# Kernel tuning notes

Measured on AMD Instinct MI355X. Metric: run time of the kernel, lower is better.

The kernel has to match this reference:

```python
import jax, jax.numpy as jnp
import numpy as np

U = 512  # units

def hard_sigmoid(x):
    # Keras hard_sigmoid: clip(0.2*x + 0.5, 0, 1)
    return jnp.clip(0.2 * x + 0.5, 0.0, 1.0)

def setup_inputs() -> dict:
    key = jax.random.key(0)
    ks = jax.random.split(key, 9)
    B, T, A, D = 64, 2048, 512, 512  # batch, annotation steps, annotation units, input dim
    s = lambda k, shape, scale: jax.random.normal(k, shape, jnp.float32) * scale
    return {
        "inputs": s(ks[0], (B, D), 1.0),
        "h": s(ks[1], (B, U), 1.0),
        "c": s(ks[2], (B, U), 1.0),
        "annotations": s(ks[3], (B, T, A), 1.0),
        "kernel": s(ks[4], (D + A, 4 * U), 0.02),
        "recurrent_kernel": s(ks[5], (U, 4 * U), 0.02),
        "bias": jnp.zeros((6 * U,), jnp.float32).at[U:2 * U].set(1.0),  # unit_forget_bias
        "kernel_u": s(ks[6], (A, U), 0.02),
        "kernel_w": s(ks[7], (U, U), 0.02),
        "kernel_v": s(ks[8], (U,), 0.02),
    }

def reference(inputs, h, c, annotations, kernel, recurrent_kernel, bias, kernel_u, kernel_w, kernel_v):
    bias_u = bias[4 * U:5 * U]
    # precomputed annotation projection (done once in build()): [B,T,U]
    uh = jnp.einsum('bta,au->btu', annotations, kernel_u) + bias_u
    # Bahdanau attention scores
    Wxstm = h @ kernel_w                                   # [B,U]
    et = jnp.einsum('btu,u->bt', jnp.tanh(uh + Wxstm[:, None, :]), kernel_v)
    at = jax.nn.softmax(et, axis=1)                        # exp/sum in source == softmax
    context = jnp.einsum('bt,bta->ba', at, annotations)    # [B,A]
    x = jnp.concatenate([inputs, context], axis=-1)        # [B, D+A]
    z = x @ kernel + h @ recurrent_kernel + bias[:4 * U]   # [B,4U]
    i = hard_sigmoid(z[:, :U])
    f = hard_sigmoid(z[:, U:2 * U])
    c_new = f * c + i * jnp.tanh(z[:, 2 * U:3 * U])
    o = hard_sigmoid(z[:, 3 * U:])
    h_new = o * jnp.tanh(c_new)
    return h_new
```

## Files before the change

kernel.cpp:

```cpp
#include <hip/hip_runtime.h>

constexpr int U = 512;
constexpr int B = 64;
constexpr int T = 2048;
constexpr int A = 512;

typedef __attribute__((ext_vector_type(8))) short short8;
typedef __attribute__((ext_vector_type(4))) float f32x4;

__device__ __forceinline__ unsigned short f32_to_bf16(float f) {
    unsigned int b = __float_as_uint(f);
    unsigned int r = (b + 0x7FFFu + ((b >> 16) & 1u)) >> 16;
    return (unsigned short)r;
}

__device__ __forceinline__ float fast_tanh(float x) {
    float e = exp2f(x * 2.885390081777927f);
    return (e - 1.0f) * __builtin_amdgcn_rcpf(e + 1.0f);
}

__device__ __forceinline__ float hard_sigmoid(float z) {
    return fminf(fmaxf(0.2f * z + 0.5f, 0.0f), 1.0f);
}

__global__ __launch_bounds__(256) void k_prep_s(const float* __restrict__ h,
                                                const float* __restrict__ kw,
                                                float* __restrict__ Sp) {
    int b = blockIdx.x >> 2;
    int kc = blockIdx.x & 3;
    int u = threadIdx.x;
    const float* hb = h + b * U + kc * 128;
    const float* kwb = kw + (size_t)kc * 128 * U;
    float a0 = 0.f, a1 = 0.f;
#pragma unroll 4
    for (int k = 0; k < 128; ++k) {
        float hv = hb[k];
        a0 += hv * kwb[(size_t)k * U + u];
        a1 += hv * kwb[(size_t)k * U + u + 256];
    }
    float* p = Sp + ((size_t)kc * 64 + b) * U;
    p[u] = a0;
    p[u + 256] = a1;
}

__global__ __launch_bounds__(256) void k_s_reduce(const float* __restrict__ Sp,
                                                  const float* __restrict__ bias,
                                                  float* __restrict__ S) {
    int gid = blockIdx.x * 256 + threadIdx.x;
    int b = gid >> 9, u = gid & 511;
    float s = bias[4 * U + u];
#pragma unroll
    for (int kc = 0; kc < 4; ++kc) s += Sp[((size_t)kc * 64 + b) * U + u];
    S[gid] = s;
}

__global__ __launch_bounds__(256) void k_prep_kpack(const float* __restrict__ ku,
                                                    unsigned short* __restrict__ kpack) {
    int t = blockIdx.x >> 1;
    int u = (blockIdx.x & 1) * 256 + threadIdx.x;
    float vals[32];
#pragma unroll
    for (int j = 0; j < 32; ++j) vals[j] = ku[(size_t)(t * 32 + j) * U + u];
    unsigned short* out = kpack + (size_t)t * 16384 + u * 32;
    int ux = (u >> 1) & 3;
#pragma unroll
    for (int d = 0; d < 4; ++d) {
        int sc = d ^ ux;
        short8 pk;
#pragma unroll
        for (int e = 0; e < 8; ++e) pk[e] = (short)f32_to_bf16(vals[d * 8 + e]);
        *(short8*)&out[sc * 8] = pk;
    }
}

__global__ __launch_bounds__(256) void k_prep_wt(const float* __restrict__ kern,
                                                 const float* __restrict__ rk,
                                                 unsigned short* __restrict__ Wt) {
    __shared__ float tile[32][33];
    int k0 = blockIdx.x << 5;
    int j0 = blockIdx.y << 5;
    int c = threadIdx.x & 31, r0 = threadIdx.x >> 5;
#pragma unroll
    for (int p = 0; p < 4; ++p) {
        int r = r0 + p * 8;
        int k = k0 + r;
        float val = (k < 1024) ? kern[k * 2048 + j0 + c]
                               : rk[(k - 1024) * 2048 + j0 + c];
        tile[r][c] = val;
    }
    __syncthreads();
#pragma unroll
    for (int p = 0; p < 4; ++p) {
        int r = r0 + p * 8;
        Wt[(size_t)(j0 + r) * 1536 + k0 + c] = f32_to_bf16(tile[c][r]);
    }
}

__global__ __launch_bounds__(256, 2) void k_gemm_et(const float* __restrict__ ann,
                                                    const unsigned short* __restrict__ kpack,
                                                    const float* __restrict__ S,
                                                    const float* __restrict__ v,
                                                    float* __restrict__ et) {
    __shared__ unsigned short As[2][64 * 32];
    __shared__ unsigned short Bs[2][512 * 32];
    __shared__ float red[4][64];

    const int tid = threadIdx.x;
    const int wave = tid >> 6;
    const int lane = tid & 63;
    const int lanelo = lane & 15;
    const int quad = lane >> 4;
    const int wn = wave;

    const int mt = blockIdx.x;
    const int b = mt >> 5;
    const int t0 = (mt & 31) << 6;
    const float* aBase = ann + (size_t)mt * 64 * A;
    const char* kpB = (const char*)kpack;

    f32x4 acc[4][8];
#pragma unroll
    for (int i = 0; i < 4; ++i)
#pragma unroll
        for (int j = 0; j < 8; ++j) acc[i][j] = {0.f, 0.f, 0.f, 0.f};

    const int rowA = tid >> 2;
    const int c8A = tid & 3;
    f32x4 pv0, pv1;

    auto stage_b = [&](int t, int buf) {
        const char* src = kpB + (size_t)t * 32768;
#pragma unroll
        for (int p = 0; p < 8; ++p) {
            int seg = p * 4 + wave;
            __builtin_amdgcn_global_load_lds(
                (const __attribute__((address_space(1))) void*)(src + seg * 1024 + lane * 16),
                (__attribute__((address_space(3))) void*)((char*)&Bs[buf][0] + seg * 1024),
                16, 0, 0);
        }
    };

    auto cvt_store = [&](int buf) {
        short8 pk;
        pk[0] = (short)f32_to_bf16(pv0.x);
        pk[1] = (short)f32_to_bf16(pv0.y);
        pk[2] = (short)f32_to_bf16(pv0.z);
        pk[3] = (short)f32_to_bf16(pv0.w);
        pk[4] = (short)f32_to_bf16(pv1.x);
        pk[5] = (short)f32_to_bf16(pv1.y);
        pk[6] = (short)f32_to_bf16(pv1.z);
        pk[7] = (short)f32_to_bf16(pv1.w);
        *(short8*)&As[buf][rowA * 32 + ((c8A ^ ((rowA >> 1) & 3)) * 8)] = pk;
    };

    {
        const float* src = aBase + (size_t)rowA * A + c8A * 8;
        pv0 = *(const f32x4*)src;
        pv1 = *(const f32x4*)(src + 4);
    }
    stage_b(0, 0);
    cvt_store(0);
    __syncthreads();

    for (int t = 0; t < 16; ++t) {
        const int cur = t & 1;
        const int nxt = cur ^ 1;
        const bool more = (t < 15);

        if (more) {
            const float* src = aBase + (size_t)rowA * A + (t + 1) * 32 + c8A * 8;
            pv0 = *(const f32x4*)src;
            pv1 = *(const f32x4*)(src + 4);
            stage_b(t + 1, nxt);
        }

        short8 af[4];
#pragma unroll
        for (int mi = 0; mi < 4; ++mi) {
            int row = mi * 16 + lanelo;
            af[mi] = *(const short8*)&As[cur][row * 32 + ((quad ^ ((row >> 1) & 3)) * 8)];
        }
        short8 bfr[8];
#pragma unroll
        for (int ni = 0; ni < 8; ++ni) {
            int rowb = wn * 128 + ni * 16 + lanelo;
            bfr[ni] = *(const short8*)&Bs[cur][rowb * 32 + ((quad ^ ((rowb >> 1) & 3)) * 8)];
        }
        __builtin_amdgcn_s_setprio(1);
#pragma unroll
        for (int mi = 0; mi < 4; ++mi)
#pragma unroll
            for (int ni = 0; ni < 8; ++ni)
                acc[mi][ni] = __builtin_amdgcn_mfma_f32_16x16x32_bf16(
                    af[mi], bfr[ni], acc[mi][ni], 0, 0, 0);
        __builtin_amdgcn_s_setprio(0);

        if (more) {
            cvt_store(nxt);
        }
        __syncthreads();
    }

    float rows[16];
#pragma unroll
    for (int i = 0; i < 16; ++i) rows[i] = 0.f;
#pragma unroll
    for (int ni = 0; ni < 8; ++ni) {
        int u = wn * 128 + ni * 16 + lanelo;
        float sv = S[b * U + u];
        float vv = v[u];
#pragma unroll
        for (int mi = 0; mi < 4; ++mi)
#pragma unroll
            for (int r = 0; r < 4; ++r)
                rows[mi * 4 + r] += fast_tanh(acc[mi][ni][r] + sv) * vv;
    }
#pragma unroll
    for (int i = 0; i < 16; ++i) {
        rows[i] += __shfl_xor(rows[i], 1);
        rows[i] += __shfl_xor(rows[i], 2);
        rows[i] += __shfl_xor(rows[i], 4);
        rows[i] += __shfl_xor(rows[i], 8);
    }
    if (lanelo == 0) {
#pragma unroll
        for (int mi = 0; mi < 4; ++mi)
#pragma unroll
            for (int r = 0; r < 4; ++r)
                red[wave][mi * 16 + quad * 4 + r] = rows[mi * 4 + r];
    }
    __syncthreads();
    if (tid < 64) {
        float sum = red[0][tid] + red[1][tid] + red[2][tid] + red[3][tid];
        et[b * T + t0 + tid] = sum;
    }
}

__global__ __launch_bounds__(256) void k_softmax(const float* __restrict__ et,
                                                 float* __restrict__ at) {
    __shared__ float sred[256];
    int b = blockIdx.x;
    const float* e = et + b * T;
    float vals[8];
    float mx = -1e30f;
#pragma unroll
    for (int i = 0; i < 8; ++i) {
        int t = threadIdx.x + i * 256;
        float x = e[t];
        vals[i] = x;
        mx = fmaxf(mx, x);
    }
    sred[threadIdx.x] = mx;
    __syncthreads();
    for (int s = 128; s > 0; s >>= 1) {
        if (threadIdx.x < s) sred[threadIdx.x] = fmaxf(sred[threadIdx.x], sred[threadIdx.x + s]);
        __syncthreads();
    }
    mx = sred[0];
    __syncthreads();
    float sum = 0.f;
#pragma unroll
    for (int i = 0; i < 8; ++i) {
        float x = exp2f((vals[i] - mx) * 1.4426950408889634f);
        vals[i] = x;
        sum += x;
    }
    sred[threadIdx.x] = sum;
    __syncthreads();
    for (int s = 128; s > 0; s >>= 1) {
        if (threadIdx.x < s) sred[threadIdx.x] += sred[threadIdx.x + s];
        __syncthreads();
    }
    float inv = 1.0f / sred[0];
#pragma unroll
    for (int i = 0; i < 8; ++i) at[b * T + threadIdx.x + i * 256] = vals[i] * inv;
}

__global__ __launch_bounds__(256) void k_ctx_part(const float* __restrict__ at,
                                                  const float* __restrict__ ann,
                                                  float* __restrict__ part) {
    __shared__ float buf[2][512];
    int b = blockIdx.x >> 4;
    int tc = blockIdx.x & 15;
    int half = threadIdx.x >> 7;
    int a4 = (threadIdx.x & 127) << 2;
    const float* annb = ann + ((size_t)b * T + tc * 128) * A;
    const float* atb = at + b * T + tc * 128;
    f32x4 acc = {0.f, 0.f, 0.f, 0.f};
#pragma unroll 4
    for (int t = half; t < 128; t += 2) {
        float w = atb[t];
        f32x4 rv = *(const f32x4*)(annb + (size_t)t * A + a4);
        acc.x += w * rv.x;
        acc.y += w * rv.y;
        acc.z += w * rv.z;
        acc.w += w * rv.w;
    }
    *(f32x4*)&buf[half][a4] = acc;
    __syncthreads();
    int a2 = threadIdx.x << 1;
    float s0 = buf[0][a2] + buf[1][a2];
    float s1 = buf[0][a2 + 1] + buf[1][a2 + 1];
    float* p = part + ((size_t)b * 16 + tc) * A;
    p[a2] = s0;
    p[a2 + 1] = s1;
}

__global__ __launch_bounds__(256) void k_ctx_xb(const float* __restrict__ part,
                                                const float* __restrict__ inputs,
                                                const float* __restrict__ h,
                                                unsigned short* __restrict__ xb) {
    int b = blockIdx.x;
    unsigned short* xrow = xb + (size_t)b * 1536;
#pragma unroll
    for (int i = 0; i < 2; ++i) {
        int a = threadIdx.x + i * 256;
        float s = 0.f;
#pragma unroll
        for (int c = 0; c < 16; ++c) s += part[((size_t)b * 16 + c) * A + a];
        xrow[512 + a] = f32_to_bf16(s);
        xrow[a] = f32_to_bf16(inputs[b * 512 + a]);
        xrow[1024 + a] = f32_to_bf16(h[b * 512 + a]);
    }
}

__global__ __launch_bounds__(256) void k_zgemm(const unsigned short* __restrict__ xb,
                                               const unsigned short* __restrict__ Wt,
                                               float* __restrict__ zpart) {
    const int kc = blockIdx.x & 7;
    const int nt = blockIdx.x >> 3;
    const int wave = threadIdx.x >> 6;
    const int lane = threadIdx.x & 63;
    const int lanelo = lane & 15;
    const int quad = lane >> 4;

    const int n = nt * 64 + wave * 16 + lanelo;
    const unsigned short* bp = Wt + (size_t)n * 1536 + kc * 192 + quad * 8;
    const unsigned short* ap = xb + (size_t)lanelo * 1536 + kc * 192 + quad * 8;

    f32x4 acc[4];
#pragma unroll
    for (int i = 0; i < 4; ++i) acc[i] = {0.f, 0.f, 0.f, 0.f};

#pragma unroll
    for (int ks = 0; ks < 6; ++ks) {
        short8 bfrag = *(const short8*)(bp + ks * 32);
#pragma unroll
        for (int mi = 0; mi < 4; ++mi) {
            short8 afrag = *(const short8*)(ap + (size_t)mi * 16 * 1536 + ks * 32);
            acc[mi] = __builtin_amdgcn_mfma_f32_16x16x32_bf16(afrag, bfrag, acc[mi], 0, 0, 0);
        }
    }

    float* p = zpart + (size_t)kc * 64 * 2048;
#pragma unroll
    for (int mi = 0; mi < 4; ++mi)
#pragma unroll
        for (int r = 0; r < 4; ++r) {
            int m = mi * 16 + quad * 4 + r;
            p[(size_t)m * 2048 + n] = acc[mi][r];
        }
}

__global__ __launch_bounds__(256) void k_gates(const float* __restrict__ zpart,
                                               const float* __restrict__ bias,
                                               const float* __restrict__ c,
                                               float* __restrict__ hnew) {
    int gid = blockIdx.x * 256 + threadIdx.x;
    int b = gid >> 9;
    int u = gid & 511;
    float z[4];
#pragma unroll
    for (int g = 0; g < 4; ++g) {
        int j = (g << 9) + u;
        float s = bias[j];
#pragma unroll
        for (int kc = 0; kc < 8; ++kc)
            s += zpart[((size_t)kc * 64 + b) * 2048 + j];
        z[g] = s;
    }
    float ig = hard_sigmoid(z[0]);
    float fg = hard_sigmoid(z[1]);
    float cn = fg * c[b * 512 + u] + ig * fast_tanh(z[2]);
    float og = hard_sigmoid(z[3]);
    hnew[b * 512 + u] = og * fast_tanh(cn);
}

extern "C" void kernel_launch(void* const* d_in, const int* in_sizes, int n_in,
                              void* d_out, int out_size, void* d_ws, size_t ws_size,
                              hipStream_t stream) {
    const float* inputs = (const float*)d_in[0];
    const float* h      = (const float*)d_in[1];
    const float* c      = (const float*)d_in[2];
    const float* ann    = (const float*)d_in[3];
    const float* kern   = (const float*)d_in[4];
    const float* rk     = (const float*)d_in[5];
    const float* bias   = (const float*)d_in[6];
    const float* ku     = (const float*)d_in[7];
    const float* kw     = (const float*)d_in[8];
    const float* kv     = (const float*)d_in[9];

    char* ws = (char*)d_ws;
    float*          S     = (float*)(ws + 0);
    unsigned short* kpack = (unsigned short*)(ws + 131072);
    float*          et    = (float*)(ws + 655360);
    float*          at    = (float*)(ws + 1703936);
    float*          Sp    = (float*)(ws + 2228224);
    unsigned short* xb    = (unsigned short*)(ws + 3407872);
    unsigned short* Wt    = (unsigned short*)(ws + 3604480);
    float*          zpart = (float*)(ws + 9895936);
    float*          part  = (float*)(ws + 14090240);
    float*          hnew  = (float*)d_out;

    k_prep_wt<<<dim3(48, 64), 256, 0, stream>>>(kern, rk, Wt);
    k_prep_kpack<<<32, 256, 0, stream>>>(ku, kpack);
    k_prep_s<<<256, 256, 0, stream>>>(h, kw, Sp);
    k_s_reduce<<<128, 256, 0, stream>>>(Sp, bias, S);
    k_gemm_et<<<2048, 256, 0, stream>>>(ann, kpack, S, kv, et);
    k_softmax<<<64, 256, 0, stream>>>(et, at);
    k_ctx_part<<<64 * 16, 256, 0, stream>>>(at, ann, part);
    k_ctx_xb<<<64, 256, 0, stream>>>(part, inputs, h, xb);
    k_zgemm<<<256, 256, 0, stream>>>(xb, Wt, zpart);
    k_gates<<<128, 256, 0, stream>>>(zpart, bias, c, hnew);
}
```

Measured before the change: 503.9 us.

## Fuse softmax and context accumulation into score GEMM via online-softmax partials

The score GEMM kernel now computes a local max and sum of exponentials for each 64-step tile. It then accumulates the exp-weighted annotation rows into a per-tile partial context while that tile is likely still in cache. This replaces the separate softmax kernel and the second full pass over annotations. A merge kernel rescales the 32 tile partials per batch with log-sum-exp weights before writing the bf16 x row. The kpack prep kernel is also spread over more blocks. The main saving is a second 256MB read of annotations and two launches. The cost is extra per-block work and a larger partial buffer.

```diff
diff --git a/kernel.cpp b/kernel.cpp
--- a/kernel.cpp
+++ b/kernel.cpp
@@ -56,21 +56,18 @@
 
 __global__ __launch_bounds__(256) void k_prep_kpack(const float* __restrict__ ku,
                                                     unsigned short* __restrict__ kpack) {
-    int t = blockIdx.x >> 1;
-    int u = (blockIdx.x & 1) * 256 + threadIdx.x;
-    float vals[32];
-#pragma unroll
-    for (int j = 0; j < 32; ++j) vals[j] = ku[(size_t)(t * 32 + j) * U + u];
-    unsigned short* out = kpack + (size_t)t * 16384 + u * 32;
-    int ux = (u >> 1) & 3;
-#pragma unroll
-    for (int d = 0; d < 4; ++d) {
-        int sc = d ^ ux;
-        short8 pk;
-#pragma unroll
-        for (int e = 0; e < 8; ++e) pk[e] = (short)f32_to_bf16(vals[d * 8 + e]);
-        *(short8*)&out[sc * 8] = pk;
-    }
+    int t = blockIdx.x >> 3;
+    int gid = (blockIdx.x & 7) * 256 + threadIdx.x;
+    int d = gid >> 9;
+    int u = gid & 511;
+    float vals[8];
+#pragma unroll
+    for (int e = 0; e < 8; ++e) vals[e] = ku[(size_t)(t * 32 + d * 8 + e) * U + u];
+    int sc = d ^ ((u >> 1) & 3);
+    short8 pk;
+#pragma unroll
+    for (int e = 0; e < 8; ++e) pk[e] = (short)f32_to_bf16(vals[e]);
+    *(short8*)&kpack[(size_t)t * 16384 + u * 32 + sc * 8] = pk;
 }
 
 __global__ __launch_bounds__(256) void k_prep_wt(const float* __restrict__ kern,
@@ -100,10 +97,12 @@
                                                     const unsigned short* __restrict__ kpack,
                                                     const float* __restrict__ S,
                                                     const float* __restrict__ v,
-                                                    float* __restrict__ et) {
+                                                    float* __restrict__ mz,
+                                                    float* __restrict__ part) {
     __shared__ unsigned short As[2][64 * 32];
     __shared__ unsigned short Bs[2][512 * 32];
     __shared__ float red[4][64];
+    __shared__ float p_lds[64];
 
     const int tid = threadIdx.x;
     const int wave = tid >> 6;
@@ -114,7 +113,6 @@
 
     const int mt = blockIdx.x;
     const int b = mt >> 5;
-    const int t0 = (mt & 31) << 6;
     const float* aBase = ann + (size_t)mt * 64 * A;
     const char* kpB = (const char*)kpack;
 
@@ -230,95 +228,81 @@
                 red[wave][mi * 16 + quad * 4 + r] = rows[mi * 4 + r];
     }
     __syncthreads();
+
     if (tid < 64) {
-        float sum = red[0][tid] + red[1][tid] + red[2][tid] + red[3][tid];
-        et[b * T + t0 + tid] = sum;
-    }
-}
-
-__global__ __launch_bounds__(256) void k_softmax(const float* __restrict__ et,
-                                                 float* __restrict__ at) {
-    __shared__ float sred[256];
+        float e = red[0][tid] + red[1][tid] + red[2][tid] + red[3][tid];
+        float m = e;
+#pragma unroll
+        for (int o = 1; o < 64; o <<= 1) m = fmaxf(m, __shfl_xor(m, o));
+        float p = exp2f((e - m) * 1.4426950408889634f);
+        float z = p;
+#pragma unroll
+        for (int o = 1; o < 64; o <<= 1) z += __shfl_xor(z, o);
+        p_lds[tid] = p;
+        if (tid == 0) { mz[mt * 2] = m; mz[mt * 2 + 1] = z; }
+    }
+    __syncthreads();
+
+    float* cbuf = (float*)&Bs[0][0];
+    {
+        int half = tid >> 7;
+        int a4 = (tid & 127) << 2;
+        f32x4 cacc = {0.f, 0.f, 0.f, 0.f};
+#pragma unroll 4
+        for (int t2 = half; t2 < 64; t2 += 2) {
+            float w = p_lds[t2];
+            f32x4 rv = *(const f32x4*)(aBase + (size_t)t2 * A + a4);
+            cacc.x += w * rv.x;
+            cacc.y += w * rv.y;
+            cacc.z += w * rv.z;
+            cacc.w += w * rv.w;
+        }
+        *(f32x4*)&cbuf[half * 512 + a4] = cacc;
+    }
+    __syncthreads();
+    {
+        int a2 = tid << 1;
+        float s0 = cbuf[a2] + cbuf[512 + a2];
+        float s1 = cbuf[a2 + 1] + cbuf[512 + a2 + 1];
+        float* p = part + (size_t)mt * 512;
+        p[a2] = s0;
+        p[a2 + 1] = s1;
+    }
+}
+
+__global__ __launch_bounds__(256) void k_ctx_merge_xb(const float* __restrict__ part,
+                                                      const float* __restrict__ mz,
+                                                      const float* __restrict__ inputs,
+                                                      const float* __restrict__ h,
+                                                      unsigned short* __restrict__ xb) {
     int b = blockIdx.x;
-    const float* e = et + b * T;
-    float vals[8];
-    float mx = -1e30f;
-#pragma unroll
-    for (int i = 0; i < 8; ++i) {
-        int t = threadIdx.x + i * 256;
-        float x = e[t];
-        vals[i] = x;
-        mx = fmaxf(mx, x);
-    }
-    sred[threadIdx.x] = mx;
-    __syncthreads();
-    for (int s = 128; s > 0; s >>= 1) {
-        if (threadIdx.x < s) sred[threadIdx.x] = fmaxf(sred[threadIdx.x], sred[threadIdx.x + s]);
-        __syncthreads();
-    }
-    mx = sred[0];
-    __syncthreads();
-    float sum = 0.f;
-#pragma unroll
-    for (int i = 0; i < 8; ++i) {
-        float x = exp2f((vals[i] - mx) * 1.4426950408889634f);
-        vals[i] = x;
-        sum += x;
-    }
-    sred[threadIdx.x] = sum;
-    __syncthreads();
-    for (int s = 128; s > 0; s >>= 1) {
-        if (threadIdx.x < s) sred[threadIdx.x] += sred[threadIdx.x + s];
-        __syncthreads();
-    }
-    float inv = 1.0f / sred[0];
-#pragma unroll
-    for (int i = 0; i < 8; ++i) at[b * T + threadIdx.x + i * 256] = vals[i] * inv;
-}
-
-__global__ __launch_bounds__(256) void k_ctx_part(const float* __restrict__ at,
-                                                  const float* __restrict__ ann,
-                                                  float* __restrict__ part) {
-    __shared__ float buf[2][512];
-    int b = blockIdx.x >> 4;
-    int tc = blockIdx.x & 15;
-    int half = threadIdx.x >> 7;
-    int a4 = (threadIdx.x & 127) << 2;
-    const float* annb = ann + ((size_t)b * T + tc * 128) * A;
-    const float* atb = at + b * T + tc * 128;
-    f32x4 acc = {0.f, 0.f, 0.f, 0.f};
-#pragma unroll 4
-    for (int t = half; t < 128; t += 2) {
-        float w = atb[t];
-        f32x4 rv = *(const f32x4*)(annb + (size_t)t * A + a4);
-        acc.x += w * rv.x;
-        acc.y += w * rv.y;
-        acc.z += w * rv.z;
-        acc.w += w * rv.w;
-    }
-    *(f32x4*)&buf[half][a4] = acc;
-    __syncthreads();
-    int a2 = threadIdx.x << 1;
-    float s0 = buf[0][a2] + buf[1][a2];
-    float s1 = buf[0][a2 + 1] + buf[1][a2 + 1];
-    float* p = part + ((size_t)b * 16 + tc) * A;
-    p[a2] = s0;
-    p[a2 + 1] = s1;
-}
-
-__global__ __launch_bounds__(256) void k_ctx_xb(const float* __restrict__ part,
-                                                const float* __restrict__ inputs,
-                                                const float* __restrict__ h,
-                                                unsigned short* __restrict__ xb) {
-    int b = blockIdx.x;
+    int tid = threadIdx.x;
+    __shared__ float wsh[32];
+    __shared__ float sinvZ;
+    if (tid < 32) {
+        float m_i = mz[(b * 32 + tid) * 2];
+        float z_i = mz[(b * 32 + tid) * 2 + 1];
+        float M = m_i;
+#pragma unroll
+        for (int o = 1; o < 32; o <<= 1) M = fmaxf(M, __shfl_xor(M, o));
+        float w = exp2f((m_i - M) * 1.4426950408889634f);
+        float wz = w * z_i;
+#pragma unroll
+        for (int o = 1; o < 32; o <<= 1) wz += __shfl_xor(wz, o);
+        wsh[tid] = w;
+        if (tid == 0) sinvZ = 1.0f / wz;
+    }
+    __syncthreads();
+    float invZ = sinvZ;
     unsigned short* xrow = xb + (size_t)b * 1536;
 #pragma unroll
     for (int i = 0; i < 2; ++i) {
-        int a = threadIdx.x + i * 256;
+        int a = tid + i * 256;
         float s = 0.f;
 #pragma unroll
-        for (int c = 0; c < 16; ++c) s += part[((size_t)b * 16 + c) * A + a];
-        xrow[512 + a] = f32_to_bf16(s);
+        for (int c2 = 0; c2 < 32; ++c2)
+            s += wsh[c2] * part[((size_t)b * 32 + c2) * 512 + a];
+        xrow[512 + a] = f32_to_bf16(s * invZ);
         xrow[a] = f32_to_bf16(inputs[b * 512 + a]);
         xrow[1024 + a] = f32_to_bf16(h[b * 512 + a]);
     }
@@ -403,23 +387,20 @@
     char* ws = (char*)d_ws;
     float*          S     = (float*)(ws + 0);
     unsigned short* kpack = (unsigned short*)(ws + 131072);
-    float*          et    = (float*)(ws + 655360);
-    float*          at    = (float*)(ws + 1703936);
-    float*          Sp    = (float*)(ws + 2228224);
-    unsigned short* xb    = (unsigned short*)(ws + 3407872);
-    unsigned short* Wt    = (unsigned short*)(ws + 3604480);
-    float*          zpart = (float*)(ws + 9895936);
-    float*          part  = (float*)(ws + 14090240);
+    float*          mz    = (float*)(ws + 655360);
+    float*          part  = (float*)(ws + 786432);
+    float*          Sp    = (float*)(ws + 4980736);
+    unsigned short* xb    = (unsigned short*)(ws + 5505024);
+    unsigned short* Wt    = (unsigned short*)(ws + 5701632);
+    float*          zpart = (float*)(ws + 11993088);
     float*          hnew  = (float*)d_out;
 
     k_prep_wt<<<dim3(48, 64), 256, 0, stream>>>(kern, rk, Wt);
-    k_prep_kpack<<<32, 256, 0, stream>>>(ku, kpack);
+    k_prep_kpack<<<128, 256, 0, stream>>>(ku, kpack);
     k_prep_s<<<256, 256, 0, stream>>>(h, kw, Sp);
     k_s_reduce<<<128, 256, 0, stream>>>(Sp, bias, S);
-    k_gemm_et<<<2048, 256, 0, stream>>>(ann, kpack, S, kv, et);
-    k_softmax<<<64, 256, 0, stream>>>(et, at);
-    k_ctx_part<<<64 * 16, 256, 0, stream>>>(at, ann, part);
-    k_ctx_xb<<<64, 256, 0, stream>>>(part, inputs, h, xb);
+    k_gemm_et<<<2048, 256, 0, stream>>>(ann, kpack, S, kv, mz, part);
+    k_ctx_merge_xb<<<64, 256, 0, stream>>>(part, mz, inputs, h, xb);
     k_zgemm<<<256, 256, 0, stream>>>(xb, Wt, zpart);
     k_gates<<<128, 256, 0, stream>>>(zpart, bias, c, hnew);
 }
```

Result: faster. 484.1 us (-3.9%).
